# Performance work log

Measured on AMD Instinct MI355X. Metric: run time of the kernel, lower is better.

## Reference

```python
import jax, jax.numpy as jnp
import numpy as np

B, C, D = 2048, 1024, 10  # batch, num_classes = 2**D leaves, num_edges = tree depth


def _build_hierarchy_buffers():
    """Balanced binary tree over C = 2**D leaves.

    Edge j (j=0 deepest, j=D-1 just below root) for leaf i corresponds to the
    ancestor of i at height j. onehot_num[i, l, j] = 1 iff leaf l is under that
    ancestor; onehot_den[i, l, j] = 1 iff leaf l is under its parent (height j+1),
    with the last column all ones (root) -- exactly what HiCE.__init__ builds.
    """
    i = np.arange(C, dtype=np.int64)[:, None, None]   # target leaf
    l = np.arange(C, dtype=np.int64)[None, :, None]   # candidate leaf
    j = np.arange(D, dtype=np.int64)[None, None, :]   # edge index (height above leaf)
    onehot_num = ((i >> j) == (l >> j)).astype(np.float32)          # [C,C,D]
    onehot_den = ((i >> (j + 1)) == (l >> (j + 1))).astype(np.float32)  # parent; j=D-1 -> all ones (root)
    heights = np.arange(D, dtype=np.float32)
    weights = np.broadcast_to(np.exp(-0.2 * heights), (C, D)).copy()  # [C,D] edge weights
    return jnp.asarray(onehot_num), jnp.asarray(onehot_den), jnp.asarray(weights)


def setup_inputs() -> dict:
    key = jax.random.key(0)
    k1, k2 = jax.random.split(key)
    inputs = jax.random.normal(k1, (B, C), dtype=jnp.float32)
    target = jax.random.randint(k2, (B,), 0, C, dtype=jnp.int64)
    onehot_num, onehot_den, weights = _build_hierarchy_buffers()
    return {"inputs": inputs, "target": target,
            "onehot_num": onehot_num, "onehot_den": onehot_den, "weights": weights}


def reference(inputs, target, onehot_num, onehot_den, weights):
    p = jax.nn.softmax(inputs, axis=1)                      # [B,C]
    num_oh = onehot_num[target]                             # [B,C,E] gather
    den_oh = onehot_den[target]                             # [B,C,E] gather
    num = jnp.einsum('bc,bce->be', p, num_oh)               # bmm([B,1,C],[B,C,E])
    den = jnp.einsum('bc,bce->be', p, den_oh)
    nz = num != 0
    # num[idx] = -log(num[idx]/den[idx]); zeros stay zero
    ratio = jnp.where(nz, num, 1.0) / jnp.where(nz, den, 1.0)
    val = jnp.where(nz, -jnp.log(ratio), 0.0)               # [B,E]
    per_sample = jnp.sum(jnp.flip(weights[target] * val, axis=1), axis=1)  # flip is sum-invariant, kept for fidelity
    return jnp.mean(per_sample)
```

## Files before the change

### kernel.cpp

```cpp
#include <hip/hip_runtime.h>


#define NB 2048
#define NC 1024
#define ND 10

__global__ __launch_bounds__(256) void hice_kernel(
    const float* __restrict__ inputs,
    const int*   __restrict__ target,
    const float* __restrict__ weights,
    float*       __restrict__ out)
{
    __shared__ float ex[NC];
    __shared__ float tree[NC - 1];
    __shared__ float wmax[4];

    const int b   = blockIdx.x;
    const int tid = threadIdx.x;
    const float* x = inputs + (size_t)b * NC;

    float v[4];
    float m = -3.402823466e38f;
#pragma unroll
    for (int i = 0; i < 4; ++i) {
        v[i] = x[tid + 256 * i];
        m = fmaxf(m, v[i]);
    }
#pragma unroll
    for (int off = 32; off > 0; off >>= 1)
        m = fmaxf(m, __shfl_xor(m, off, 64));
    if ((tid & 63) == 0) wmax[tid >> 6] = m;
    __syncthreads();
    m = fmaxf(fmaxf(wmax[0], wmax[1]), fmaxf(wmax[2], wmax[3]));

#pragma unroll
    for (int i = 0; i < 4; ++i)
        ex[tid + 256 * i] = expf(v[i] - m);
    __syncthreads();

    for (int i = tid; i < 512; i += 256)
        tree[i] = ex[2 * i] + ex[2 * i + 1];
    __syncthreads();
#pragma unroll
    for (int e = 2; e <= ND; ++e) {
        const int n = NC >> e;
        const float* src = tree + (NC - (1 << (12 - e)));
        float*       dst = tree + (NC - (1 << (11 - e)));
        if (tid < n) dst[tid] = src[2 * tid] + src[2 * tid + 1];
        __syncthreads();
    }

    if (tid == 0) {
        const int t = target[b];
        const float* wrow = weights + (size_t)t * ND;
        float S_prev = ex[t];
        float loss = 0.0f;
#pragma unroll
        for (int e = 1; e <= ND; ++e) {
            const float S_cur = tree[NC - (1 << (11 - e)) + (t >> e)];
            if (S_prev != 0.0f)
                loss += wrow[e - 1] * (-logf(S_prev / S_cur));
            S_prev = S_cur;
        }
        atomicAdd(out, loss * (1.0f / NB));
    }
}

extern "C" void kernel_launch(void* const* d_in, const int* in_sizes, int n_in,
                              void* d_out, int out_size, void* d_ws, size_t ws_size,
                              hipStream_t stream)
{
    const float* inputs  = (const float*)d_in[0];
    const int*   target  = (const int*)d_in[1];
    const float* weights = (const float*)d_in[4];
    float* out = (float*)d_out;

    hipMemsetAsync(out, 0, sizeof(float), stream);
    hice_kernel<<<NB, 256, 0, stream>>>(inputs, target, weights, out);
}
```

Before: 135.0 us.

## Map one wavefront per sample and replace shared-memory tree with shuffle sums

Each 64-lane wavefront now handles a whole sample with float4 loads. Subtree sums are built in registers for the lowest four levels and with xor-shuffles for the upper six, which removes the shared-memory tree and its many block barriers. The single atomic accumulation and the memset are replaced by per-block partials in the workspace plus a second single-block reduction kernel. The cost is an extra kernel launch, and it relies on the workspace holding the partials.

```diff
diff --git a/kernel.cpp b/kernel.cpp
--- a/kernel.cpp
+++ b/kernel.cpp
@@ -4,66 +4,96 @@
 #define NB 2048
 #define NC 1024
 #define ND 10
+#define WPB 4
+#define GRID1 (NB / WPB)
 
-__global__ __launch_bounds__(256) void hice_kernel(
+__global__ __launch_bounds__(256) void hice_stage1(
     const float* __restrict__ inputs,
     const int*   __restrict__ target,
     const float* __restrict__ weights,
-    float*       __restrict__ out)
+    float*       __restrict__ partial)
 {
-    __shared__ float ex[NC];
-    __shared__ float tree[NC - 1];
-    __shared__ float wmax[4];
+    const int tid  = threadIdx.x;
+    const int w    = tid >> 6;
+    const int lane = tid & 63;
+    const int b    = blockIdx.x * WPB + w;
 
-    const int b   = blockIdx.x;
-    const int tid = threadIdx.x;
-    const float* x = inputs + (size_t)b * NC;
+    const float4* x4 = (const float4*)(inputs + (size_t)b * NC);
 
-    float v[4];
-    float m = -3.402823466e38f;
+    float4 q0 = x4[lane * 4 + 0];
+    float4 q1 = x4[lane * 4 + 1];
+    float4 q2 = x4[lane * 4 + 2];
+    float4 q3 = x4[lane * 4 + 3];
+    float v[16] = {q0.x,q0.y,q0.z,q0.w, q1.x,q1.y,q1.z,q1.w,
+                   q2.x,q2.y,q2.z,q2.w, q3.x,q3.y,q3.z,q3.w};
+
+    float m = v[0];
 #pragma unroll
-    for (int i = 0; i < 4; ++i) {
-        v[i] = x[tid + 256 * i];
-        m = fmaxf(m, v[i]);
-    }
+    for (int i = 1; i < 16; ++i) m = fmaxf(m, v[i]);
 #pragma unroll
     for (int off = 32; off > 0; off >>= 1)
         m = fmaxf(m, __shfl_xor(m, off, 64));
-    if ((tid & 63) == 0) wmax[tid >> 6] = m;
-    __syncthreads();
-    m = fmaxf(fmaxf(wmax[0], wmax[1]), fmaxf(wmax[2], wmax[3]));
 
+    float s = 0.0f;
 #pragma unroll
-    for (int i = 0; i < 4; ++i)
-        ex[tid + 256 * i] = expf(v[i] - m);
-    __syncthreads();
-
-    for (int i = tid; i < 512; i += 256)
-        tree[i] = ex[2 * i] + ex[2 * i + 1];
-    __syncthreads();
-#pragma unroll
-    for (int e = 2; e <= ND; ++e) {
-        const int n = NC >> e;
-        const float* src = tree + (NC - (1 << (12 - e)));
-        float*       dst = tree + (NC - (1 << (11 - e)));
-        if (tid < n) dst[tid] = src[2 * tid] + src[2 * tid + 1];
-        __syncthreads();
+    for (int i = 0; i < 16; ++i) {
+        v[i] = expf(v[i] - m);
+        s += v[i];
     }
 
-    if (tid == 0) {
-        const int t = target[b];
-        const float* wrow = weights + (size_t)t * ND;
-        float S_prev = ex[t];
-        float loss = 0.0f;
+    const int t = target[b];
+    const int j = t & 15;
+
+    float S0 = 0.f, S1 = 0.f, S2 = 0.f, S3 = 0.f;
 #pragma unroll
-        for (int e = 1; e <= ND; ++e) {
-            const float S_cur = tree[NC - (1 << (11 - e)) + (t >> e)];
-            if (S_prev != 0.0f)
-                loss += wrow[e - 1] * (-logf(S_prev / S_cur));
-            S_prev = S_cur;
-        }
-        atomicAdd(out, loss * (1.0f / NB));
+    for (int i = 0; i < 16; ++i) {
+        S0 += (i == j)               ? v[i] : 0.f;
+        S1 += ((i >> 1) == (j >> 1)) ? v[i] : 0.f;
+        S2 += ((i >> 2) == (j >> 2)) ? v[i] : 0.f;
+        S3 += ((i >> 3) == (j >> 3)) ? v[i] : 0.f;
     }
+
+    float S[ND + 1];
+    S[0] = S0; S[1] = S1; S[2] = S2; S[3] = S3; S[4] = s;
+    float cur = s;
+#pragma unroll
+    for (int d = 0; d < 6; ++d) {
+        cur += __shfl_xor(cur, 1 << d, 64);
+        S[5 + d] = cur;
+    }
+
+    const float* wrow = weights + (size_t)t * ND;
+    float loss = 0.0f;
+#pragma unroll
+    for (int e = 1; e <= ND; ++e) {
+        const float Sp = S[e - 1], Sc = S[e];
+        const bool nz = (Sp != 0.0f);
+        const float r = (nz ? Sp : 1.0f) / (nz ? Sc : 1.0f);
+        loss += nz ? wrow[e - 1] * (-logf(r)) : 0.0f;
+    }
+    loss = __shfl(loss, t >> 4, 64);
+
+    __shared__ float wloss[WPB];
+    if (lane == 0) wloss[w] = loss;
+    __syncthreads();
+    if (tid == 0)
+        partial[blockIdx.x] = wloss[0] + wloss[1] + wloss[2] + wloss[3];
+}
+
+__global__ __launch_bounds__(256) void hice_stage2(
+    const float* __restrict__ partial,
+    float*       __restrict__ out)
+{
+    const int tid = threadIdx.x;
+    float s = partial[tid] + partial[tid + 256];
+#pragma unroll
+    for (int off = 32; off > 0; off >>= 1)
+        s += __shfl_xor(s, off, 64);
+    __shared__ float ws[4];
+    if ((tid & 63) == 0) ws[tid >> 6] = s;
+    __syncthreads();
+    if (tid == 0)
+        out[0] = (ws[0] + ws[1] + ws[2] + ws[3]) * (1.0f / NB);
 }
 
 extern "C" void kernel_launch(void* const* d_in, const int* in_sizes, int n_in,
@@ -73,8 +103,9 @@
     const float* inputs  = (const float*)d_in[0];
     const int*   target  = (const int*)d_in[1];
     const float* weights = (const float*)d_in[4];
+    float* partial = (float*)d_ws;
     float* out = (float*)d_out;
 
-    hipMemsetAsync(out, 0, sizeof(float), stream);
-    hice_kernel<<<NB, 256, 0, stream>>>(inputs, target, weights, out);
+    hice_stage1<<<GRID1, 256, 0, stream>>>(inputs, target, weights, partial);
+    hice_stage2<<<1, 256, 0, stream>>>(partial, out);
 }
```

After: 111.2 us. 17.6% less time.
